# Performance work log

Hardware: AMD Instinct MI355X
Metric: run time of the kernel (lower is better)

Reference implementation:

```python
import jax, jax.numpy as jnp
import numpy as np

EPS = 1e-16

def _householder_cascade(vectors):
    # vectors: [N, S, 1]
    v = vectors[..., 0]                                  # [N, S]
    outer = jnp.einsum('ns,nt->nst', v, v)               # [N, S, S]
    inner = jnp.sum(v * v, axis=-1)[:, None, None]       # [N, 1, 1]
    S = v.shape[-1]
    I = jnp.eye(S, dtype=vectors.dtype)
    hh = I[None] - 2.0 * outer / (inner + EPS)           # [N, S, S]
    # sequential left-to-right product: Q = H_0 @ H_1 @ ... @ H_{N-1}
    def step(Q, M):
        return Q @ M, None
    Q, _ = jax.lax.scan(step, I, hh)
    return Q

def setup_inputs() -> dict:
    key = jax.random.key(0)
    k1, k2 = jax.random.split(key)
    S, N, B = 256, 258, 65536
    vectors = jax.random.normal(k1, (N, S, 1), dtype=jnp.float32)
    vectors = vectors / jnp.linalg.norm(vectors, axis=1, keepdims=True)
    x = jax.random.normal(k2, (B, S), dtype=jnp.float32)
    return {"x": x, "vectors": vectors}

def reference(x, vectors):
    Q = _householder_cascade(vectors)   # [S, S]
    return x @ Q.T
```

## Files before the change

### kernel.cpp

```cpp
#include <hip/hip_runtime.h>


#define GLOAD_LDS16(g, l)                                                      \
  __builtin_amdgcn_global_load_lds(                                            \
      (const __attribute__((address_space(1))) void*)(g),                      \
      (__attribute__((address_space(3))) void*)(l), 16, 0, 0)

typedef __attribute__((ext_vector_type(8))) short bf16x8;
typedef __attribute__((ext_vector_type(4))) float f32x4;

__device__ __forceinline__ unsigned short f2bf_rne(float f) {
  unsigned u = __builtin_bit_cast(unsigned, f);
  return (unsigned short)((u + 0x7fffu + ((u >> 16) & 1u)) >> 16);
}

struct bfpair { short hi, lo; };

__device__ __forceinline__ bfpair bf_split(float x) {
  unsigned short hu = f2bf_rne(x);
  float hf = __builtin_bit_cast(float, (unsigned)hu << 16);
  bfpair r;
  r.hi = (short)hu;
  r.lo = (short)f2bf_rne(x - hf);
  return r;
}

template <int CTRL>
__device__ __forceinline__ float dpp_add(float v) {
  int t = __builtin_amdgcn_update_dpp(0, __builtin_bit_cast(int, v), CTRL, 0xF,
                                      0xF, true);
  return v + __builtin_bit_cast(float, t);
}

__global__ void hh_scale(const float* __restrict__ vecs, float* __restrict__ u) {
  const int n = blockIdx.x;
  const int l = threadIdx.x;
  float4* uo = (float4*)(u + (long)n * 256) + l;
  if (n >= 258) {
    *uo = make_float4(0.f, 0.f, 0.f, 0.f);
    return;
  }
  const float4 v = *((const float4*)(vecs + (long)n * 256) + l);
  float p = v.x * v.x + v.y * v.y + v.z * v.z + v.w * v.w;
#pragma unroll
  for (int off = 32; off; off >>= 1) p += __shfl_xor(p, off);
  const float s = sqrtf(2.0f / (p + 1e-16f));
  *uo = make_float4(v.x * s, v.y * s, v.z * s, v.w * s);
}

__launch_bounds__(64, 1)
__global__ void hh_qchunk(const float* __restrict__ u,
                          float* __restrict__ Qc,
                          float* __restrict__ QcT) {
  const int l = threadIdx.x;
  const int chunk = blockIdx.x >> 6;
  const int rg = blockIdx.x & 63;
  const int r = l >> 4;
  const int c = l & 15;
  const int row = rg * 4 + r;
  const int col0 = c * 16;

  float q[16];
#pragma unroll
  for (int i = 0; i < 16; ++i) q[i] = (col0 + i == row) ? 1.f : 0.f;

  const float* ub = u + (long)chunk * 33 * 256 + col0;

  auto load16 = [&](float(&d)[16], int n) {
    const float4* v = (const float4*)(ub + (long)n * 256);
#pragma unroll
    for (int i = 0; i < 4; ++i) {
      float4 t = v[i];
      d[4 * i] = t.x; d[4 * i + 1] = t.y; d[4 * i + 2] = t.z; d[4 * i + 3] = t.w;
    }
  };

  auto step = [&](const float(&a)[16]) {
    float p0 = 0.f, p1 = 0.f, p2 = 0.f, p3 = 0.f;
#pragma unroll
    for (int e = 0; e < 4; ++e) {
      p0 = fmaf(q[e], a[e], p0);
      p1 = fmaf(q[4 + e], a[4 + e], p1);
      p2 = fmaf(q[8 + e], a[8 + e], p2);
      p3 = fmaf(q[12 + e], a[12 + e], p3);
    }
    float p = (p0 + p1) + (p2 + p3);
    p = dpp_add<0xB1>(p);
    p = dpp_add<0x4E>(p);
    p = dpp_add<0x124>(p);
    p = dpp_add<0x128>(p);
#pragma unroll
    for (int k = 0; k < 16; ++k) q[k] = fmaf(-p, a[k], q[k]);
  };

  float A0[16], A1[16];
  load16(A0, 0);
  load16(A1, 1);
  for (int n = 0; n < 32; n += 2) {
    step(A0);
    load16(A0, n + 2);
    step(A1);
    load16(A1, n + 3);
  }
  step(A0);

  float4* out = (float4*)(Qc + (long)chunk * 65536 + row * 256 + col0);
#pragma unroll
  for (int i = 0; i < 4; ++i)
    out[i] = make_float4(q[4 * i], q[4 * i + 1], q[4 * i + 2], q[4 * i + 3]);
  float* outT = QcT + (long)chunk * 65536 + row;
#pragma unroll
  for (int i = 0; i < 16; ++i) outT[(col0 + i) * 256] = q[i];
}

__launch_bounds__(64)
__global__ void hh_merge(const float* __restrict__ A0,
                         const float* __restrict__ BT0,
                         float* __restrict__ C0, float* __restrict__ CT0,
                         unsigned short* __restrict__ outb, int to_bf16) {
  const int p = blockIdx.x >> 6;
  const int t = blockIdx.x & 63;
  const int ti = (t >> 3) * 32, tj = (t & 7) * 32;
  const int lane = threadIdx.x;
  const int fr = lane & 15, fg = lane >> 4;
  const float* A = A0 + (long)p * 2 * 65536;
  const float* BT = BT0 + (long)p * 2 * 65536 + 65536;

  f32x4 acc[2][2];
#pragma unroll
  for (int m = 0; m < 2; ++m)
#pragma unroll
    for (int n = 0; n < 2; ++n) acc[m][n] = (f32x4){0.f, 0.f, 0.f, 0.f};

  for (int kt = 0; kt < 8; ++kt) {
    const int k0 = kt * 32 + fg * 8;
    bf16x8 ahi[2], alo[2], bhi[2], blo[2];
#pragma unroll
    for (int m = 0; m < 2; ++m) {
      const float* ap = A + (long)(ti + m * 16 + fr) * 256 + k0;
      f32x4 x0 = *(const f32x4*)ap;
      f32x4 x1 = *(const f32x4*)(ap + 4);
#pragma unroll
      for (int e = 0; e < 4; ++e) {
        bfpair p0 = bf_split(x0[e]);
        bfpair p1 = bf_split(x1[e]);
        ahi[m][e] = p0.hi; alo[m][e] = p0.lo;
        ahi[m][4 + e] = p1.hi; alo[m][4 + e] = p1.lo;
      }
    }
#pragma unroll
    for (int n = 0; n < 2; ++n) {
      const float* bp = BT + (long)(tj + n * 16 + fr) * 256 + k0;
      f32x4 x0 = *(const f32x4*)bp;
      f32x4 x1 = *(const f32x4*)(bp + 4);
#pragma unroll
      for (int e = 0; e < 4; ++e) {
        bfpair p0 = bf_split(x0[e]);
        bfpair p1 = bf_split(x1[e]);
        bhi[n][e] = p0.hi; blo[n][e] = p0.lo;
        bhi[n][4 + e] = p1.hi; blo[n][4 + e] = p1.lo;
      }
    }
#pragma unroll
    for (int m = 0; m < 2; ++m)
#pragma unroll
      for (int n = 0; n < 2; ++n) {
        acc[m][n] = __builtin_amdgcn_mfma_f32_16x16x32_bf16(ahi[m], bhi[n],
                                                            acc[m][n], 0, 0, 0);
        acc[m][n] = __builtin_amdgcn_mfma_f32_16x16x32_bf16(ahi[m], blo[n],
                                                            acc[m][n], 0, 0, 0);
        acc[m][n] = __builtin_amdgcn_mfma_f32_16x16x32_bf16(alo[m], bhi[n],
                                                            acc[m][n], 0, 0, 0);
      }
  }

#pragma unroll
  for (int m = 0; m < 2; ++m)
#pragma unroll
    for (int n = 0; n < 2; ++n)
#pragma unroll
      for (int rr = 0; rr < 4; ++rr) {
        const int grow = ti + m * 16 + fg * 4 + rr;
        const int gcol = tj + n * 16 + fr;
        const float val = acc[m][n][rr];
        if (to_bf16) {
          outb[grow * 256 + gcol] = f2bf_rne(val);
        } else {
          C0[(long)p * 65536 + grow * 256 + gcol] = val;
          CT0[(long)p * 65536 + gcol * 256 + grow] = val;
        }
      }
}

__launch_bounds__(512)
__global__ void hh_gemm(const float* __restrict__ X,
                        const unsigned short* __restrict__ Qb,
                        float* __restrict__ Y) {
  __shared__ __align__(128) char lds[65536];
  const int tid = threadIdx.x;
  const int lane = tid & 63;
  const int wid = tid >> 6;
  const int wm = wid >> 2;
  const int wn = wid & 3;
  const int fr = lane & 15;
  const int fg = lane >> 4;
  const long bm0 = (long)blockIdx.x * 128;

  auto stage = [&](int buf, int kt) {
#pragma unroll
    for (int r2 = 0; r2 < 2; ++r2) {
      int slot = r2 * 512 + tid;
      int row = slot >> 3, seg = slot & 7;
      int ps = seg ^ (row & 7);
      GLOAD_LDS16(X + (bm0 + row) * 256 + kt * 32 + ps * 4,
                  lds + buf * 16384 + slot * 16);
    }
#pragma unroll
    for (int r2 = 0; r2 < 2; ++r2) {
      int slot = r2 * 512 + tid;
      int row = slot >> 2, seg = slot & 3;
      int ps = seg ^ (row & 3);
      GLOAD_LDS16(Qb + row * 256 + kt * 32 + ps * 8,
                  lds + 32768 + buf * 16384 + slot * 16);
    }
  };

  f32x4 acc[4][4];
#pragma unroll
  for (int m = 0; m < 4; ++m)
#pragma unroll
    for (int n = 0; n < 4; ++n) acc[m][n] = (f32x4){0.f, 0.f, 0.f, 0.f};

  stage(0, 0);
  __syncthreads();

  for (int kt = 0; kt < 8; ++kt) {
    const int cur = kt & 1;
    if (kt < 7) stage(cur ^ 1, kt + 1);

    bf16x8 aF[4], bF[4];
#pragma unroll
    for (int m = 0; m < 4; ++m) {
      int row = wm * 64 + m * 16 + fr;
      int s0 = (2 * fg) ^ (row & 7);
      int s1 = (2 * fg + 1) ^ (row & 7);
      const f32x4 x0 = *(const f32x4*)(lds + cur * 16384 + row * 128 + s0 * 16);
      const f32x4 x1 = *(const f32x4*)(lds + cur * 16384 + row * 128 + s1 * 16);
      bf16x8 t;
      t[0] = (short)f2bf_rne(x0[0]);
      t[1] = (short)f2bf_rne(x0[1]);
      t[2] = (short)f2bf_rne(x0[2]);
      t[3] = (short)f2bf_rne(x0[3]);
      t[4] = (short)f2bf_rne(x1[0]);
      t[5] = (short)f2bf_rne(x1[1]);
      t[6] = (short)f2bf_rne(x1[2]);
      t[7] = (short)f2bf_rne(x1[3]);
      aF[m] = t;
    }
#pragma unroll
    for (int n = 0; n < 4; ++n) {
      int row = wn * 64 + n * 16 + fr;
      int ps = fg ^ (row & 3);
      bF[n] = *(const bf16x8*)(lds + 32768 + cur * 16384 + row * 64 + ps * 16);
    }
#pragma unroll
    for (int m = 0; m < 4; ++m)
#pragma unroll
      for (int n = 0; n < 4; ++n)
        acc[m][n] =
            __builtin_amdgcn_mfma_f32_16x16x32_bf16(aF[m], bF[n], acc[m][n], 0, 0, 0);
    __syncthreads();
  }

#pragma unroll
  for (int m = 0; m < 4; ++m)
#pragma unroll
    for (int n = 0; n < 4; ++n)
#pragma unroll
      for (int r = 0; r < 4; ++r) {
        long grow = bm0 + wm * 64 + m * 16 + fg * 4 + r;
        int gcol = wn * 64 + n * 16 + fr;
        Y[grow * 256 + gcol] = acc[m][n][r];
      }
}

extern "C" void kernel_launch(void* const* d_in, const int* in_sizes, int n_in,
                              void* d_out, int out_size, void* d_ws, size_t ws_size,
                              hipStream_t stream) {
  const float* x = (const float*)d_in[0];
  const float* vecs = (const float*)d_in[1];
  float* y = (float*)d_out;

  char* ws = (char*)d_ws;
  float* u = (float*)ws;
  unsigned short* Qb = (unsigned short*)(ws + 278528);

  char* ob = (char*)d_out;
  float* Qc  = (float*)(ob);
  float* QcT = (float*)(ob + 2097152);
  float* P   = (float*)(ob + 4194304);
  float* PT  = (float*)(ob + 5242880);
  float* R   = (float*)(ob + 6291456);
  float* RT  = (float*)(ob + 6815744);

  hh_scale<<<272, 64, 0, stream>>>(vecs, u);
  hh_qchunk<<<512, 64, 0, stream>>>(u, Qc, QcT);
  hh_merge<<<256, 64, 0, stream>>>(Qc, QcT, P, PT, nullptr, 0);
  hh_merge<<<128, 64, 0, stream>>>(P, PT, R, RT, nullptr, 0);
  hh_merge<<<64, 64, 0, stream>>>(R, RT, nullptr, nullptr, Qb, 1);
  hh_gemm<<<512, 512, 0, stream>>>(x, Qb, y);
}
```

Before: 71.09 us.

## Fuse Householder scaling, chunk products and merges into one cooperative kernel

```diff
diff --git a/kernel.cpp b/kernel.cpp
--- a/kernel.cpp
+++ b/kernel.cpp
@@ -1,4 +1,7 @@
 #include <hip/hip_runtime.h>
+#include <hip/hip_cooperative_groups.h>
+
+namespace cg = cooperative_groups;
 
 
 #define GLOAD_LDS16(g, l)                                                      \
@@ -32,99 +35,22 @@
   return v + __builtin_bit_cast(float, t);
 }
 
-__global__ void hh_scale(const float* __restrict__ vecs, float* __restrict__ u) {
-  const int n = blockIdx.x;
-  const int l = threadIdx.x;
-  float4* uo = (float4*)(u + (long)n * 256) + l;
-  if (n >= 258) {
-    *uo = make_float4(0.f, 0.f, 0.f, 0.f);
-    return;
-  }
-  const float4 v = *((const float4*)(vecs + (long)n * 256) + l);
-  float p = v.x * v.x + v.y * v.y + v.z * v.z + v.w * v.w;
-#pragma unroll
-  for (int off = 32; off; off >>= 1) p += __shfl_xor(p, off);
-  const float s = sqrtf(2.0f / (p + 1e-16f));
-  *uo = make_float4(v.x * s, v.y * s, v.z * s, v.w * s);
-}
-
-__launch_bounds__(64, 1)
-__global__ void hh_qchunk(const float* __restrict__ u,
-                          float* __restrict__ Qc,
-                          float* __restrict__ QcT) {
-  const int l = threadIdx.x;
-  const int chunk = blockIdx.x >> 6;
-  const int rg = blockIdx.x & 63;
-  const int r = l >> 4;
-  const int c = l & 15;
-  const int row = rg * 4 + r;
-  const int col0 = c * 16;
-
-  float q[16];
-#pragma unroll
-  for (int i = 0; i < 16; ++i) q[i] = (col0 + i == row) ? 1.f : 0.f;
-
-  const float* ub = u + (long)chunk * 33 * 256 + col0;
-
-  auto load16 = [&](float(&d)[16], int n) {
-    const float4* v = (const float4*)(ub + (long)n * 256);
-#pragma unroll
-    for (int i = 0; i < 4; ++i) {
-      float4 t = v[i];
-      d[4 * i] = t.x; d[4 * i + 1] = t.y; d[4 * i + 2] = t.z; d[4 * i + 3] = t.w;
-    }
-  };
-
-  auto step = [&](const float(&a)[16]) {
-    float p0 = 0.f, p1 = 0.f, p2 = 0.f, p3 = 0.f;
-#pragma unroll
-    for (int e = 0; e < 4; ++e) {
-      p0 = fmaf(q[e], a[e], p0);
-      p1 = fmaf(q[4 + e], a[4 + e], p1);
-      p2 = fmaf(q[8 + e], a[8 + e], p2);
-      p3 = fmaf(q[12 + e], a[12 + e], p3);
-    }
-    float p = (p0 + p1) + (p2 + p3);
-    p = dpp_add<0xB1>(p);
-    p = dpp_add<0x4E>(p);
-    p = dpp_add<0x124>(p);
-    p = dpp_add<0x128>(p);
-#pragma unroll
-    for (int k = 0; k < 16; ++k) q[k] = fmaf(-p, a[k], q[k]);
-  };
-
-  float A0[16], A1[16];
-  load16(A0, 0);
-  load16(A1, 1);
-  for (int n = 0; n < 32; n += 2) {
-    step(A0);
-    load16(A0, n + 2);
-    step(A1);
-    load16(A1, n + 3);
-  }
-  step(A0);
-
-  float4* out = (float4*)(Qc + (long)chunk * 65536 + row * 256 + col0);
-#pragma unroll
-  for (int i = 0; i < 4; ++i)
-    out[i] = make_float4(q[4 * i], q[4 * i + 1], q[4 * i + 2], q[4 * i + 3]);
-  float* outT = QcT + (long)chunk * 65536 + row;
-#pragma unroll
-  for (int i = 0; i < 16; ++i) outT[(col0 + i) * 256] = q[i];
-}
-
-__launch_bounds__(64)
-__global__ void hh_merge(const float* __restrict__ A0,
-                         const float* __restrict__ BT0,
-                         float* __restrict__ C0, float* __restrict__ CT0,
-                         unsigned short* __restrict__ outb, int to_bf16) {
-  const int p = blockIdx.x >> 6;
-  const int t = blockIdx.x & 63;
+__device__ __forceinline__ float dpp_sum16(float p) {
+  p = dpp_add<0xB1>(p);
+  p = dpp_add<0x4E>(p);
+  p = dpp_add<0x124>(p);
+  p = dpp_add<0x128>(p);
+  return p;
+}
+
+__device__ __forceinline__ void merge_tile(const float* __restrict__ A,
+                                           const float* __restrict__ BT,
+                                           float* __restrict__ C,
+                                           float* __restrict__ CT,
+                                           unsigned short* __restrict__ outb,
+                                           int t, int lane) {
   const int ti = (t >> 3) * 32, tj = (t & 7) * 32;
-  const int lane = threadIdx.x;
   const int fr = lane & 15, fg = lane >> 4;
-  const float* A = A0 + (long)p * 2 * 65536;
-  const float* BT = BT0 + (long)p * 2 * 65536 + 65536;
 
   f32x4 acc[2][2];
 #pragma unroll
@@ -183,13 +109,126 @@
         const int grow = ti + m * 16 + fg * 4 + rr;
         const int gcol = tj + n * 16 + fr;
         const float val = acc[m][n][rr];
-        if (to_bf16) {
+        if (outb) {
           outb[grow * 256 + gcol] = f2bf_rne(val);
         } else {
-          C0[(long)p * 65536 + grow * 256 + gcol] = val;
-          CT0[(long)p * 65536 + gcol * 256 + grow] = val;
+          C[grow * 256 + gcol] = val;
+          CT[gcol * 256 + grow] = val;
         }
       }
+}
+
+__launch_bounds__(64, 1)
+__global__ void hh_fused(const float* __restrict__ vecs,
+                         float* __restrict__ Qc, float* __restrict__ QcT,
+                         float* __restrict__ P, float* __restrict__ PT,
+                         float* __restrict__ R, float* __restrict__ RT,
+                         unsigned short* __restrict__ Qb) {
+  cg::grid_group grid = cg::this_grid();
+  const int b = blockIdx.x;
+  const int l = threadIdx.x;
+
+  {
+    const int chunk = b >> 6;
+    const int rg = b & 63;
+    const int r = l >> 4;
+    const int cl = l & 15;
+    const int row = rg * 4 + r;
+    const int col0 = cl * 16;
+    const int brow = chunk * 33;
+
+    __shared__ float cs[36];
+
+    for (int n = r; n < 36; n += 4) {
+      const int gr = brow + n;
+      const int grc = gr > 257 ? 257 : gr;
+      const float4* vp = (const float4*)(vecs + (long)grc * 256 + col0);
+      float s = 0.f;
+#pragma unroll
+      for (int i = 0; i < 4; ++i) {
+        float4 t = vp[i];
+        s += t.x * t.x + t.y * t.y + t.z * t.z + t.w * t.w;
+      }
+      s = dpp_sum16(s);
+      if (cl == 0) cs[n] = (n < 33 && gr < 258) ? 2.0f / (s + 1e-16f) : 0.f;
+    }
+    __syncthreads();
+
+    float q[16];
+#pragma unroll
+    for (int i = 0; i < 16; ++i) q[i] = (col0 + i == row) ? 1.f : 0.f;
+
+    auto load16 = [&](float(&d)[16], int n) {
+      const int gr = brow + n;
+      const int grc = gr > 257 ? 257 : gr;
+      const float4* v = (const float4*)(vecs + (long)grc * 256 + col0);
+#pragma unroll
+      for (int i = 0; i < 4; ++i) {
+        float4 t = v[i];
+        d[4 * i] = t.x; d[4 * i + 1] = t.y;
+        d[4 * i + 2] = t.z; d[4 * i + 3] = t.w;
+      }
+    };
+
+    auto step = [&](const float(&a)[16], float cc) {
+      float p0 = 0.f, p1 = 0.f, p2 = 0.f, p3 = 0.f;
+#pragma unroll
+      for (int e = 0; e < 4; ++e) {
+        p0 = fmaf(q[e], a[e], p0);
+        p1 = fmaf(q[4 + e], a[4 + e], p1);
+        p2 = fmaf(q[8 + e], a[8 + e], p2);
+        p3 = fmaf(q[12 + e], a[12 + e], p3);
+      }
+      const float p = dpp_sum16((p0 + p1) + (p2 + p3));
+      const float s = cc * p;
+#pragma unroll
+      for (int k = 0; k < 16; ++k) q[k] = fmaf(-s, a[k], q[k]);
+    };
+
+    float A0[16], A1[16];
+    load16(A0, 0);
+    load16(A1, 1);
+    float c0 = cs[0], c1 = cs[1];
+    for (int n = 0; n < 32; n += 2) {
+      const float cn0 = cs[n + 2], cn1 = cs[n + 3];
+      step(A0, c0);
+      load16(A0, n + 2);
+      step(A1, c1);
+      load16(A1, n + 3);
+      c0 = cn0; c1 = cn1;
+    }
+    step(A0, c0);
+
+    float4* out = (float4*)(Qc + (long)chunk * 65536 + row * 256 + col0);
+#pragma unroll
+    for (int i = 0; i < 4; ++i)
+      out[i] = make_float4(q[4 * i], q[4 * i + 1], q[4 * i + 2], q[4 * i + 3]);
+    float* outT = QcT + (long)chunk * 65536 + row;
+#pragma unroll
+    for (int i = 0; i < 16; ++i) outT[(col0 + i) * 256] = q[i];
+  }
+
+  grid.sync();
+
+  if (b < 256) {
+    const int p = b >> 6, t = b & 63;
+    merge_tile(Qc + (long)p * 2 * 65536, QcT + (long)p * 2 * 65536 + 65536,
+               P + (long)p * 65536, PT + (long)p * 65536, nullptr, t, l);
+  }
+
+  grid.sync();
+
+  if (b < 128) {
+    const int p = b >> 6, t = b & 63;
+    merge_tile(P + (long)p * 2 * 65536, PT + (long)p * 2 * 65536 + 65536,
+               R + (long)p * 65536, RT + (long)p * 65536, nullptr, t, l);
+  }
+
+  grid.sync();
+
+  if (b < 64) {
+    merge_tile(R, RT + 65536, nullptr, nullptr, Qb, b, l);
+  }
 }
 
 __launch_bounds__(512)
@@ -291,22 +330,19 @@
   const float* vecs = (const float*)d_in[1];
   float* y = (float*)d_out;
 
-  char* ws = (char*)d_ws;
-  float* u = (float*)ws;
-  unsigned short* Qb = (unsigned short*)(ws + 278528);
+  unsigned short* Qb = (unsigned short*)d_ws;
 
   char* ob = (char*)d_out;
-  float* Qc  = (float*)(ob);
+  float* Qc = (float*)(ob);
   float* QcT = (float*)(ob + 2097152);
-  float* P   = (float*)(ob + 4194304);
-  float* PT  = (float*)(ob + 5242880);
-  float* R   = (float*)(ob + 6291456);
-  float* RT  = (float*)(ob + 6815744);
-
-  hh_scale<<<272, 64, 0, stream>>>(vecs, u);
-  hh_qchunk<<<512, 64, 0, stream>>>(u, Qc, QcT);
-  hh_merge<<<256, 64, 0, stream>>>(Qc, QcT, P, PT, nullptr, 0);
-  hh_merge<<<128, 64, 0, stream>>>(P, PT, R, RT, nullptr, 0);
-  hh_merge<<<64, 64, 0, stream>>>(R, RT, nullptr, nullptr, Qb, 1);
+  float* P = (float*)(ob + 4194304);
+  float* PT = (float*)(ob + 5242880);
+  float* R = (float*)(ob + 6291456);
+  float* RT = (float*)(ob + 6815744);
+
+  void* args[] = {(void*)&vecs, (void*)&Qc, (void*)&QcT, (void*)&P,
+                  (void*)&PT,   (void*)&R,  (void*)&RT,  (void*)&Qb};
+  hipLaunchCooperativeKernel((void*)hh_fused, dim3(512), dim3(64), args, 0,
+                             stream);
   hh_gemm<<<512, 512, 0, stream>>>(x, Qb, y);
 }
```

After: 244.1 us. 243% more time.
